# Performance work log

Measured on AMD Instinct MI355X. Metric: run time of the kernel, lower is better.

The kernel has to match this reference:

```python
import jax, jax.numpy as jnp
import numpy as np

B, S, I, H = 256, 512, 512, 1024


def setup_inputs() -> dict:
    key = jax.random.key(0)
    ks = jax.random.split(key, 7)
    s = 1.0 / np.sqrt(H)
    x = jax.random.normal(ks[0], (B, S, I), jnp.float32)
    # equinox GRUCell params: weight_ih (3H,I), weight_hh (3H,H), bias (3H,), bias_n (H,)
    wi = jax.random.uniform(ks[1], (3 * H, I), jnp.float32, -s, s)
    wh = jax.random.uniform(ks[2], (3 * H, H), jnp.float32, -s, s)
    bi = jax.random.uniform(ks[3], (3 * H,), jnp.float32, -s, s)
    bn = jax.random.uniform(ks[4], (H,), jnp.float32, -s, s)
    # final Linear(H, 1)
    sl = 1.0 / np.sqrt(H)
    wl = jax.random.uniform(ks[5], (1, H), jnp.float32, -sl, sl)
    bl = jax.random.uniform(ks[6], (1,), jnp.float32, -sl, sl)
    return {"x": x, "wi": wi, "wh": wh, "bi": bi, "bn": bn, "wl": wl, "bl": bl}


def reference(x, wi, wh, bi, bn, wl, bl):
    # x: (B, S, I). Precompute input-side gate projections for all timesteps
    # (same math as per-step wi @ x_t + bi, hoisted out of the scan).
    ig_all = jnp.einsum('bsi,gi->sbg', x, wi) + bi  # (S, B, 3H)

    def step(h, ig_t):
        hg = h @ wh.T  # (B, 3H)
        ir, iz, ia = jnp.split(ig_t, 3, axis=-1)
        hr, hz, ha = jnp.split(hg, 3, axis=-1)
        r = jax.nn.sigmoid(ir + hr)          # reset gate
        z = jax.nn.sigmoid(iz + hz)          # update gate (equinox 'inp')
        n = jnp.tanh(ia + r * (ha + bn))     # candidate (uses bias_n)
        h_new = n + z * (h - n)              # equinox GRUCell output
        return h_new, None

    h0 = jnp.zeros((x.shape[0], wh.shape[1]), x.dtype)
    hT, _ = jax.lax.scan(step, h0, ig_all)
    energies = hT @ wl.T + bl  # (B, 1)
    return jnp.squeeze(energies, axis=-1)  # (B,)
```

## Files before the change

### kernel.cpp

```cpp
#include <hip/hip_runtime.h>
#include <hip/hip_bf16.h>


#define B_  256
#define S_  512
#define I_  512
#define H_  1024
#define GSIZE 64

typedef __bf16 bf16x8 __attribute__((ext_vector_type(8)));
typedef float  f32x4  __attribute__((ext_vector_type(4)));

union U16x8 { int4 i; bf16x8 b; unsigned short s[8]; unsigned u[4]; };

__device__ __forceinline__ unsigned pack2bf(float lo, float hi) {
    union { float f; unsigned u; } a, b;
    a.f = lo; b.f = hi;
    return __builtin_amdgcn_perm(b.u + 0x8000u, a.u + 0x8000u, 0x07060302u);
}
__device__ __forceinline__ unsigned short f2bf1(float f) {
    union { float f; unsigned u; } v; v.f = f;
    return (unsigned short)((v.u + 0x8000u) >> 16);
}
__device__ __forceinline__ bf16x8 ldb(const unsigned short* p) {
    U16x8 u; u.i = *(const int4*)p; return u.b;
}
__device__ __forceinline__ bf16x8 ldh_dev(const unsigned long long* p) {
    unsigned long long lo = __hip_atomic_load(p,     __ATOMIC_RELAXED, __HIP_MEMORY_SCOPE_AGENT);
    unsigned long long hi = __hip_atomic_load(p + 1, __ATOMIC_RELAXED, __HIP_MEMORY_SCOPE_AGENT);
    union { unsigned long long q[2]; bf16x8 b; } u;
    u.q[0] = lo; u.q[1] = hi; return u.b;
}

__global__ void prep_kernel(const float* __restrict__ wh, const float* __restrict__ wi,
                            unsigned* __restrict__ hbA_u, unsigned* __restrict__ whb_u,
                            unsigned* __restrict__ wib_u, unsigned* __restrict__ flags) {
    int idx = blockIdx.x * blockDim.x + threadIdx.x;
    int stride = gridDim.x * blockDim.x;
    const float2* wh2 = (const float2*)wh;
    const float2* wi2 = (const float2*)wi;
    for (int i = idx; i < 3 * H_ * H_ / 2; i += stride) { float2 v = wh2[i]; whb_u[i] = pack2bf(v.x, v.y); }
    for (int i = idx; i < 3 * H_ * I_ / 2; i += stride) { float2 v = wi2[i]; wib_u[i] = pack2bf(v.x, v.y); }
    for (int i = idx; i < B_ * H_ / 2; i += stride) hbA_u[i] = 0u;
    if (idx < 256 * 16) flags[idx] = 0u;
}

__global__ __launch_bounds__(256, 1) void gru_persistent(
    const float* __restrict__ x,
    const unsigned short* __restrict__ whb,
    const unsigned short* __restrict__ wib,
    const float* __restrict__ bi,
    const float* __restrict__ bn,
    unsigned short* __restrict__ hbufA,
    unsigned short* __restrict__ hbufB,
    float* __restrict__ h32g,
    unsigned* __restrict__ flags)
{
    __shared__ float partial[4 * 3 * 16 * 68];
    __shared__ float h32s[64 * 17];

    const int tid  = threadIdx.x;
    const int w    = tid >> 6;
    const int lane = tid & 63;
    const int col  = lane & 15;
    const int quad = lane >> 4;

    const int hblk = blockIdx.x & 63;
    const int mt   = blockIdx.x >> 6;
    const int k0   = hblk << 4;
    const int b0   = mt << 6;
    const int kwh  = w << 8;
    const int kwi  = w << 7;

    bf16x8 Bh[3][8];
    bf16x8 Bx[3][4];
    #pragma unroll
    for (int g = 0; g < 3; ++g) {
        const unsigned short* bh = whb + ((size_t)(g * H_ + k0 + col)) * H_ + kwh + (quad << 3);
        #pragma unroll
        for (int kk = 0; kk < 8; ++kk) Bh[g][kk] = ldb(bh + kk * 32);
        const unsigned short* bx = wib + ((size_t)(g * H_ + k0 + col)) * I_ + kwi + (quad << 3);
        #pragma unroll
        for (int kk = 0; kk < 4; ++kk) Bx[g][kk] = ldb(bx + kk * 32);
    }

    const int hcol = k0 + col;
    const float bir = bi[hcol], biz = bi[H_ + hcol], bia = bi[2 * H_ + hcol], bnv = bn[hcol];

    for (int i = tid; i < 64 * 17; i += 256) h32s[i] = 0.f;
    __syncthreads();

    unsigned* myflag = flags + blockIdx.x * 16;
    const unsigned* grpflags = flags + (mt * 64) * 16;

    const f32x4 zero4 = {0.f, 0.f, 0.f, 0.f};

    for (int t = 0; t < S_; ++t) {
        f32x4 acc[4][4];
        #pragma unroll
        for (int mi = 0; mi < 4; ++mi)
            #pragma unroll
            for (int j = 0; j < 4; ++j) acc[mi][j] = zero4;

        const float* xbase = x + ((size_t)(b0 + col) * S_ + (size_t)t) * I_ + kwi + (quad << 3);
        #pragma unroll
        for (int kk = 0; kk < 4; ++kk) {
            #pragma unroll
            for (int mi = 0; mi < 4; ++mi) {
                const float* p = xbase + (size_t)mi * 16 * S_ * I_ + kk * 32;
                float4 f0 = *(const float4*)p;
                float4 f1 = *(const float4*)(p + 4);
                U16x8 u;
                u.u[0] = pack2bf(f0.x, f0.y);
                u.u[1] = pack2bf(f0.z, f0.w);
                u.u[2] = pack2bf(f1.x, f1.y);
                u.u[3] = pack2bf(f1.z, f1.w);
                bf16x8 a = u.b;
                acc[mi][0] = __builtin_amdgcn_mfma_f32_16x16x32_bf16(a, Bx[0][kk], acc[mi][0], 0, 0, 0);
                acc[mi][1] = __builtin_amdgcn_mfma_f32_16x16x32_bf16(a, Bx[1][kk], acc[mi][1], 0, 0, 0);
                acc[mi][2] = __builtin_amdgcn_mfma_f32_16x16x32_bf16(a, Bx[2][kk], acc[mi][2], 0, 0, 0);
            }
        }

        if (t > 0) {
            if (w == 0) {
                const unsigned* fp = grpflags + lane * 16;
                while (__hip_atomic_load(fp, __ATOMIC_RELAXED, __HIP_MEMORY_SCOPE_AGENT) < (unsigned)t)
                    __builtin_amdgcn_s_sleep(1);
            }
            __syncthreads();
        }

        const unsigned short* hcur = (t & 1) ? hbufB : hbufA;
        const unsigned short* hrow = hcur + (size_t)(b0 + col) * H_ + kwh + (quad << 3);
        #pragma unroll
        for (int kk = 0; kk < 8; ++kk) {
            #pragma unroll
            for (int mi = 0; mi < 4; ++mi) {
                bf16x8 a = ldh_dev((const unsigned long long*)(hrow + (size_t)mi * 16 * H_ + kk * 32));
                acc[mi][0] = __builtin_amdgcn_mfma_f32_16x16x32_bf16(a, Bh[0][kk], acc[mi][0], 0, 0, 0);
                acc[mi][1] = __builtin_amdgcn_mfma_f32_16x16x32_bf16(a, Bh[1][kk], acc[mi][1], 0, 0, 0);
                acc[mi][3] = __builtin_amdgcn_mfma_f32_16x16x32_bf16(a, Bh[2][kk], acc[mi][3], 0, 0, 0);
            }
        }

        #pragma unroll
        for (int mi = 0; mi < 4; ++mi) {
            if (mi == w) continue;
            int slot = mi - (mi > w ? 1 : 0);
            float* dst = partial + (size_t)((w * 3 + slot) * 16) * 68;
            #pragma unroll
            for (int j = 0; j < 4; ++j)
                #pragma unroll
                for (int r = 0; r < 4; ++r)
                    dst[((quad << 2) + r) * 68 + j * 16 + col] = acc[mi][j][r];
        }
        __syncthreads();

        unsigned short* hnext = (t & 1) ? hbufA : hbufB;
        #pragma unroll
        for (int r = 0; r < 4; ++r) {
            float sr = 0.f, sz = 0.f, sia = 0.f, sha = 0.f;
            #pragma unroll
            for (int mi = 0; mi < 4; ++mi)
                if (mi == w) { sr = acc[mi][0][r]; sz = acc[mi][1][r]; sia = acc[mi][2][r]; sha = acc[mi][3][r]; }
            #pragma unroll
            for (int p = 0; p < 4; ++p) {
                if (p == w) continue;
                int slot = w - (w > p ? 1 : 0);
                const float* src = partial + (size_t)(((p * 3 + slot) * 16 + (quad << 2) + r)) * 68 + col;
                sr  += src[0];
                sz  += src[16];
                sia += src[32];
                sha += src[48];
            }
            float rg = 1.f / (1.f + __expf(-(sr + bir)));
            float zg = 1.f / (1.f + __expf(-(sz + biz)));
            float pa = sia + bia + rg * (sha + bnv);
            float e2 = __expf(2.f * pa);
            float ng = 1.f - 2.f / (e2 + 1.f);
            int m = (w << 4) + (quad << 2) + r;
            float hold = h32s[m * 17 + col];
            float hnew = ng + zg * (hold - ng);
            h32s[m * 17 + col] = hnew;
            size_t off = (size_t)(b0 + m) * H_ + k0 + col;
            __hip_atomic_store(hnext + off, f2bf1(hnew), __ATOMIC_RELAXED, __HIP_MEMORY_SCOPE_AGENT);
            if (t == S_ - 1) h32g[off] = hnew;
        }

        __syncthreads();
        if (tid == 0)
            __hip_atomic_store(myflag, (unsigned)(t + 1), __ATOMIC_RELAXED, __HIP_MEMORY_SCOPE_AGENT);
    }
}

__global__ __launch_bounds__(256) void final_kernel(const float* __restrict__ h32,
                                                    const float* __restrict__ wl,
                                                    const float* __restrict__ bl,
                                                    float* __restrict__ out) {
    const int b = blockIdx.x;
    float s = 0.f;
    for (int k = threadIdx.x; k < H_; k += 256)
        s += h32[((size_t)b << 10) + k] * wl[k];
    #pragma unroll
    for (int off = 32; off > 0; off >>= 1)
        s += __shfl_down(s, off, 64);
    __shared__ float red[4];
    const int wave = threadIdx.x >> 6;
    const int lane = threadIdx.x & 63;
    if (lane == 0) red[wave] = s;
    __syncthreads();
    if (threadIdx.x == 0)
        out[b] = red[0] + red[1] + red[2] + red[3] + bl[0];
}

extern "C" void kernel_launch(void* const* d_in, const int* in_sizes, int n_in,
                              void* d_out, int out_size, void* d_ws, size_t ws_size,
                              hipStream_t stream) {
    const float* x  = (const float*)d_in[0];
    const float* wi = (const float*)d_in[1];
    const float* wh = (const float*)d_in[2];
    const float* bi = (const float*)d_in[3];
    const float* bn = (const float*)d_in[4];
    const float* wl = (const float*)d_in[5];
    const float* bl = (const float*)d_in[6];
    float* out = (float*)d_out;

    char* ws = (char*)d_ws;
    float*          h32g  = (float*)ws;
    unsigned short* hbA   = (unsigned short*)(ws + (1u << 20));
    unsigned short* hbB   = (unsigned short*)(ws + (1u << 20) + (512u << 10));
    unsigned short* whb   = (unsigned short*)(ws + (2u << 20));
    unsigned short* wib   = (unsigned short*)(ws + (8u << 20));
    unsigned*       flags = (unsigned*)(ws + (11u << 20));

    prep_kernel<<<1024, 256, 0, stream>>>(wh, wi, (unsigned*)hbA, (unsigned*)whb, (unsigned*)wib, flags);
    gru_persistent<<<256, 256, 0, stream>>>(x, whb, wib, bi, bn, hbA, hbB, h32g, flags);
    final_kernel<<<B_, 256, 0, stream>>>(h32g, wl, bl, out);
}
```

Measured before the change: 9.316 ms.

## Pre-convert x to bf16, per-wave flag polling, and packed 64-bit h stores

```diff
diff --git a/kernel.cpp b/kernel.cpp
--- a/kernel.cpp
+++ b/kernel.cpp
@@ -18,10 +18,6 @@
     a.f = lo; b.f = hi;
     return __builtin_amdgcn_perm(b.u + 0x8000u, a.u + 0x8000u, 0x07060302u);
 }
-__device__ __forceinline__ unsigned short f2bf1(float f) {
-    union { float f; unsigned u; } v; v.f = f;
-    return (unsigned short)((v.u + 0x8000u) >> 16);
-}
 __device__ __forceinline__ bf16x8 ldb(const unsigned short* p) {
     U16x8 u; u.i = *(const int4*)p; return u.b;
 }
@@ -33,8 +29,10 @@
 }
 
 __global__ void prep_kernel(const float* __restrict__ wh, const float* __restrict__ wi,
+                            const float* __restrict__ x,
                             unsigned* __restrict__ hbA_u, unsigned* __restrict__ whb_u,
-                            unsigned* __restrict__ wib_u, unsigned* __restrict__ flags) {
+                            unsigned* __restrict__ wib_u, unsigned* __restrict__ flags,
+                            unsigned* __restrict__ xb_u) {
     int idx = blockIdx.x * blockDim.x + threadIdx.x;
     int stride = gridDim.x * blockDim.x;
     const float2* wh2 = (const float2*)wh;
@@ -43,10 +41,17 @@
     for (int i = idx; i < 3 * H_ * I_ / 2; i += stride) { float2 v = wi2[i]; wib_u[i] = pack2bf(v.x, v.y); }
     for (int i = idx; i < B_ * H_ / 2; i += stride) hbA_u[i] = 0u;
     if (idx < 256 * 16) flags[idx] = 0u;
-}
-
+    if (xb_u) {
+        const float2* x2 = (const float2*)x;
+        const int n = B_ * S_ * I_ / 2;
+        for (int i = idx; i < n; i += stride) { float2 v = x2[i]; xb_u[i] = pack2bf(v.x, v.y); }
+    }
+}
+
+template<int XB>
 __global__ __launch_bounds__(256, 1) void gru_persistent(
     const float* __restrict__ x,
+    const unsigned short* __restrict__ xbp,
     const unsigned short* __restrict__ whb,
     const unsigned short* __restrict__ wib,
     const float* __restrict__ bi,
@@ -102,33 +107,47 @@
             #pragma unroll
             for (int j = 0; j < 4; ++j) acc[mi][j] = zero4;
 
-        const float* xbase = x + ((size_t)(b0 + col) * S_ + (size_t)t) * I_ + kwi + (quad << 3);
-        #pragma unroll
-        for (int kk = 0; kk < 4; ++kk) {
-            #pragma unroll
-            for (int mi = 0; mi < 4; ++mi) {
-                const float* p = xbase + (size_t)mi * 16 * S_ * I_ + kk * 32;
-                float4 f0 = *(const float4*)p;
-                float4 f1 = *(const float4*)(p + 4);
-                U16x8 u;
-                u.u[0] = pack2bf(f0.x, f0.y);
-                u.u[1] = pack2bf(f0.z, f0.w);
-                u.u[2] = pack2bf(f1.x, f1.y);
-                u.u[3] = pack2bf(f1.z, f1.w);
-                bf16x8 a = u.b;
-                acc[mi][0] = __builtin_amdgcn_mfma_f32_16x16x32_bf16(a, Bx[0][kk], acc[mi][0], 0, 0, 0);
-                acc[mi][1] = __builtin_amdgcn_mfma_f32_16x16x32_bf16(a, Bx[1][kk], acc[mi][1], 0, 0, 0);
-                acc[mi][2] = __builtin_amdgcn_mfma_f32_16x16x32_bf16(a, Bx[2][kk], acc[mi][2], 0, 0, 0);
+        if constexpr (XB) {
+            const unsigned short* xbase = xbp + ((size_t)(b0 + col) * S_ + (size_t)t) * I_ + kwi + (quad << 3);
+            #pragma unroll
+            for (int kk = 0; kk < 4; ++kk) {
+                #pragma unroll
+                for (int mi = 0; mi < 4; ++mi) {
+                    bf16x8 a = ldb(xbase + (size_t)mi * 16 * S_ * I_ + kk * 32);
+                    acc[mi][0] = __builtin_amdgcn_mfma_f32_16x16x32_bf16(a, Bx[0][kk], acc[mi][0], 0, 0, 0);
+                    acc[mi][1] = __builtin_amdgcn_mfma_f32_16x16x32_bf16(a, Bx[1][kk], acc[mi][1], 0, 0, 0);
+                    acc[mi][2] = __builtin_amdgcn_mfma_f32_16x16x32_bf16(a, Bx[2][kk], acc[mi][2], 0, 0, 0);
+                }
+            }
+        } else {
+            const float* xbase = x + ((size_t)(b0 + col) * S_ + (size_t)t) * I_ + kwi + (quad << 3);
+            #pragma unroll
+            for (int kk = 0; kk < 4; ++kk) {
+                #pragma unroll
+                for (int mi = 0; mi < 4; ++mi) {
+                    const float* p = xbase + (size_t)mi * 16 * S_ * I_ + kk * 32;
+                    float4 f0 = *(const float4*)p;
+                    float4 f1 = *(const float4*)(p + 4);
+                    U16x8 u;
+                    u.u[0] = pack2bf(f0.x, f0.y);
+                    u.u[1] = pack2bf(f0.z, f0.w);
+                    u.u[2] = pack2bf(f1.x, f1.y);
+                    u.u[3] = pack2bf(f1.z, f1.w);
+                    bf16x8 a = u.b;
+                    acc[mi][0] = __builtin_amdgcn_mfma_f32_16x16x32_bf16(a, Bx[0][kk], acc[mi][0], 0, 0, 0);
+                    acc[mi][1] = __builtin_amdgcn_mfma_f32_16x16x32_bf16(a, Bx[1][kk], acc[mi][1], 0, 0, 0);
+                    acc[mi][2] = __builtin_amdgcn_mfma_f32_16x16x32_bf16(a, Bx[2][kk], acc[mi][2], 0, 0, 0);
+                }
             }
         }
 
         if (t > 0) {
-            if (w == 0) {
-                const unsigned* fp = grpflags + lane * 16;
+            if (lane < 16) {
+                const unsigned* fp = grpflags + (((w << 4) + lane) << 4);
                 while (__hip_atomic_load(fp, __ATOMIC_RELAXED, __HIP_MEMORY_SCOPE_AGENT) < (unsigned)t)
                     __builtin_amdgcn_s_sleep(1);
             }
-            __syncthreads();
+            asm volatile("" ::: "memory");
         }
 
         const unsigned short* hcur = (t & 1) ? hbufB : hbufA;
@@ -157,7 +176,6 @@
         }
         __syncthreads();
 
-        unsigned short* hnext = (t & 1) ? hbufA : hbufB;
         #pragma unroll
         for (int r = 0; r < 4; ++r) {
             float sr = 0.f, sz = 0.f, sia = 0.f, sha = 0.f;
@@ -183,12 +201,22 @@
             float hold = h32s[m * 17 + col];
             float hnew = ng + zg * (hold - ng);
             h32s[m * 17 + col] = hnew;
-            size_t off = (size_t)(b0 + m) * H_ + k0 + col;
-            __hip_atomic_store(hnext + off, f2bf1(hnew), __ATOMIC_RELAXED, __HIP_MEMORY_SCOPE_AGENT);
-            if (t == S_ - 1) h32g[off] = hnew;
-        }
-
+            if (t == S_ - 1) h32g[(size_t)(b0 + m) * H_ + k0 + col] = hnew;
+        }
         __syncthreads();
+
+        {
+            unsigned short* hnext = (t & 1) ? hbufA : hbufB;
+            const int m  = tid >> 2;
+            const int c4 = (tid & 3) << 2;
+            const float* hp = h32s + m * 17 + c4;
+            unsigned long long pkt = (unsigned long long)pack2bf(hp[0], hp[1])
+                                   | ((unsigned long long)pack2bf(hp[2], hp[3]) << 32);
+            __hip_atomic_store((unsigned long long*)(hnext + (size_t)(b0 + m) * H_ + k0 + c4),
+                               pkt, __ATOMIC_RELAXED, __HIP_MEMORY_SCOPE_AGENT);
+        }
+        __syncthreads();
+
         if (tid == 0)
             __hip_atomic_store(myflag, (unsigned)(t + 1), __ATOMIC_RELAXED, __HIP_MEMORY_SCOPE_AGENT);
     }
@@ -233,8 +261,14 @@
     unsigned short* whb   = (unsigned short*)(ws + (2u << 20));
     unsigned short* wib   = (unsigned short*)(ws + (8u << 20));
     unsigned*       flags = (unsigned*)(ws + (11u << 20));
-
-    prep_kernel<<<1024, 256, 0, stream>>>(wh, wi, (unsigned*)hbA, (unsigned*)whb, (unsigned*)wib, flags);
-    gru_persistent<<<256, 256, 0, stream>>>(x, whb, wib, bi, bn, hbA, hbB, h32g, flags);
+    const bool use_xb = ws_size >= (145ull << 20);
+    unsigned short* xbw = use_xb ? (unsigned short*)(ws + (16ull << 20)) : nullptr;
+
+    prep_kernel<<<1024, 256, 0, stream>>>(wh, wi, x, (unsigned*)hbA, (unsigned*)whb,
+                                          (unsigned*)wib, flags, (unsigned*)xbw);
+    if (use_xb)
+        gru_persistent<1><<<256, 256, 0, stream>>>(x, xbw, whb, wib, bi, bn, hbA, hbB, h32g, flags);
+    else
+        gru_persistent<0><<<256, 256, 0, stream>>>(x, nullptr, whb, wib, bi, bn, hbA, hbB, h32g, flags);
     final_kernel<<<B_, 256, 0, stream>>>(h32g, wl, bl, out);
 }
```

Result: faster. 8.280 ms (-11.1%).
